# Optimization experiments

Measured on AMD Instinct MI355X. Metric: run time of the kernel, lower is better.

## Reference

```python
import jax, jax.numpy as jnp
import numpy as np

N, E = 50000, 800000          # nodes, edges (avg degree 16)
NFEAT, NHID, NCLASS = 256, 128, 64
HEADS = 4
P_DROP = 0.5


def setup_inputs() -> dict:
    key = jax.random.key(0)
    ks = jax.random.split(key, 12)

    def w(k, shape, fan_in):
        return jax.random.normal(k, shape, jnp.float32) * (1.0 / np.sqrt(fan_in))

    return {
        "features": jax.random.normal(ks[0], (N, NFEAT), jnp.float32),
        "src": jax.random.randint(ks[1], (E,), 0, N, jnp.int32),
        "dst": jax.random.randint(ks[2], (E,), 0, N, jnp.int32),
        # gc1: nfeat->nhid, 3 layers
        "wqkv1_0": w(ks[3], (3, NFEAT, NHID), NFEAT),
        "wqkv1_r": w(ks[4], (2, 3, NHID, NHID), NHID),
        "wo1": w(ks[5], (3, NHID, NHID), NHID),
        # gc2: nhid->nclass, 3 layers
        "wqkv2_0": w(ks[6], (3, NHID, NCLASS), NHID),
        "wqkv2_r": w(ks[7], (2, 3, NCLASS, NCLASS), NCLASS),
        "wo2": w(ks[8], (3, NCLASS, NCLASS), NCLASS),
        # gc3: nhid->nclass, 3 layers
        "wqkv3_0": w(ks[9], (3, NHID, NCLASS), NHID),
        "wqkv3_r": w(ks[10], (2, 3, NCLASS, NCLASS), NCLASS),
        "wo3": w(ks[11], (3, NCLASS, NCLASS), NCLASS),
    }


def _l2norm(x):
    # F.normalize(x): L2 along dim 1, eps=1e-12
    n = jnp.sqrt(jnp.sum(x * x, axis=1, keepdims=True))
    return x / jnp.maximum(n, 1e-12)


def _graph_transformer(h, src, dst, wqkv0, wqkvr, wo):
    """Stacked graph-transformer layers: gather q[dst]/k[src], edge-softmax per dst, scatter-sum v."""
    n = h.shape[0]
    n_layers = wo.shape[0]
    for l in range(n_layers):  # fixed small structural loop
        w = wqkv0 if l == 0 else wqkvr[l - 1]
        out_dim = w.shape[2]
        dh = out_dim // HEADS
        q = (h @ w[0]).reshape(n, HEADS, dh)
        k = (h @ w[1]).reshape(n, HEADS, dh)
        v = (h @ w[2]).reshape(n, HEADS, dh)
        # per-edge attention scores [E, H]
        s = jnp.einsum('ehd,ehd->eh', q[dst], k[src]) / np.sqrt(dh).astype(np.float32)
        # edge softmax over incoming edges of each dst node
        m = jax.ops.segment_max(s, dst, num_segments=n)
        e = jnp.exp(s - m[dst])
        denom = jax.ops.segment_sum(e, dst, num_segments=n)
        alpha = e / denom[dst]
        agg = jax.ops.segment_sum(alpha[:, :, None] * v[src], dst, num_segments=n)
        h = agg.reshape(n, out_dim) @ wo[l]
        if l < n_layers - 1:
            h = jax.nn.relu(h)
    return h


def reference(features, src, dst, wqkv1_0, wqkv1_r, wo1,
              wqkv2_0, wqkv2_r, wo2, wqkv3_0, wqkv3_r, wo3):
    key = jax.random.key(42)
    kd, ke = jax.random.split(key)

    x = _graph_transformer(features, src, dst, wqkv1_0, wqkv1_r, wo1)
    x = jax.nn.relu(_l2norm(x))
    # dropout (training=True), deterministic key
    keep = jax.random.bernoulli(kd, 1.0 - P_DROP, x.shape)
    x = jnp.where(keep, x / (1.0 - P_DROP), 0.0)

    mu = _l2norm(_graph_transformer(x, src, dst, wqkv2_0, wqkv2_r, wo2))
    logvar = _l2norm(_graph_transformer(x, src, dst, wqkv3_0, wqkv3_r, wo3))

    # reparameterize (training): std = exp(logvar) + 1e-12 (matches source exactly)
    std = jnp.exp(logvar) + 1e-12
    eps = jax.random.normal(ke, std.shape, std.dtype)
    z = eps * std + mu
    return z
```

## Files before the change

### kernel.cpp

```cpp
#include <hip/hip_runtime.h>
#include <stdint.h>
#include <math.h>

#define NN 50000
#define NE 800000
#define NH 4

typedef __attribute__((ext_vector_type(8))) short short8;
typedef __attribute__((ext_vector_type(4))) float floatx4;

__device__ inline float bf2f(uint32_t u16)
{
    return __uint_as_float(u16 << 16);
}
__device__ inline uint16_t f2bf(float f)
{
    uint32_t u = __float_as_uint(f);
    uint32_t r = (u + 0x7fffu + ((u >> 16) & 1u)) >> 16;
    return (uint16_t)r;
}
__device__ inline void unpk8(uint4 u, float* f)
{
    f[0] = bf2f(u.x & 0xffffu); f[1] = bf2f(u.x >> 16);
    f[2] = bf2f(u.y & 0xffffu); f[3] = bf2f(u.y >> 16);
    f[4] = bf2f(u.z & 0xffffu); f[5] = bf2f(u.z >> 16);
    f[6] = bf2f(u.w & 0xffffu); f[7] = bf2f(u.w >> 16);
}

__device__ inline void wave_lds_sync()
{
    __builtin_amdgcn_wave_barrier();
    asm volatile("s_waitcnt lgkmcnt(0)" ::: "memory");
    __builtin_amdgcn_wave_barrier();
}

__host__ __device__ inline void tf2x32(uint32_t k0, uint32_t k1,
                                       uint32_t x0, uint32_t x1,
                                       uint32_t& o0, uint32_t& o1)
{
    uint32_t ks2 = k0 ^ k1 ^ 0x1BD11BDAu;
    x0 += k0; x1 += k1;
#define TF_R(r) { x0 += x1; x1 = (x1 << (r)) | (x1 >> (32 - (r))); x1 ^= x0; }
    TF_R(13) TF_R(15) TF_R(26) TF_R(6)
    x0 += k1;  x1 += ks2 + 1u;
    TF_R(17) TF_R(29) TF_R(16) TF_R(24)
    x0 += ks2; x1 += k0 + 2u;
    TF_R(13) TF_R(15) TF_R(26) TF_R(6)
    x0 += k0;  x1 += k1 + 3u;
    TF_R(17) TF_R(29) TF_R(16) TF_R(24)
    x0 += k1;  x1 += ks2 + 4u;
    TF_R(13) TF_R(15) TF_R(26) TF_R(6)
    x0 += ks2; x1 += k0 + 5u;
#undef TF_R
    o0 = x0; o1 = x1;
}

__device__ inline uint32_t jax_bits32(uint32_t k0, uint32_t k1, uint32_t idx)
{
    uint32_t a, b;
    tf2x32(k0, k1, 0u, idx, a, b);
    return a ^ b;
}

__device__ inline float jax_u01(uint32_t bits)
{
    return __uint_as_float((bits >> 9) | 0x3f800000u) - 1.0f;
}

__device__ inline float erfinv_f(float x)
{
    float w = -log1pf(-x * x);
    float p;
    if (w < 5.0f) {
        w = w - 2.5f;
        p = 2.81022636e-08f;
        p = fmaf(p, w, 3.43273939e-07f);
        p = fmaf(p, w, -3.5233877e-06f);
        p = fmaf(p, w, -4.39150654e-06f);
        p = fmaf(p, w, 0.00021858087f);
        p = fmaf(p, w, -0.00125372503f);
        p = fmaf(p, w, -0.00417768164f);
        p = fmaf(p, w, 0.246640727f);
        p = fmaf(p, w, 1.50140941f);
    } else {
        w = sqrtf(w) - 3.0f;
        p = -0.000200214257f;
        p = fmaf(p, w, 0.000100950558f);
        p = fmaf(p, w, 0.00134934322f);
        p = fmaf(p, w, -0.00367342844f);
        p = fmaf(p, w, 0.00573950773f);
        p = fmaf(p, w, -0.0076224613f);
        p = fmaf(p, w, 0.00943887047f);
        p = fmaf(p, w, 1.00167406f);
        p = fmaf(p, w, 2.83297682f);
    }
    return p * x;
}

__global__ __launch_bounds__(256) void fill_u32_k(uint32_t* p, uint32_t v, int n)
{
    int i = blockIdx.x * blockDim.x + threadIdx.x;
    if (i < n) p[i] = v;
}

__global__ __launch_bounds__(256) void f2bf_vec_k(const float* __restrict__ in,
                                                  uint16_t* __restrict__ out, int n)
{
    int i = (blockIdx.x * blockDim.x + threadIdx.x) * 4;
    if (i >= n) return;
    float4 v = *(const float4*)(in + i);
    out[i + 0] = f2bf(v.x); out[i + 1] = f2bf(v.y);
    out[i + 2] = f2bf(v.z); out[i + 3] = f2bf(v.w);
}

struct WSeg { const float* src; int B, K, C, off; };
struct WSegs { WSeg s[18]; };

__global__ __launch_bounds__(256) void wconv_k(WSegs segs, uint16_t* __restrict__ Wt)
{
    WSeg sg = segs.s[blockIdx.y];
    int n = sg.B * sg.K * sg.C;
    int i = blockIdx.x * 256 + threadIdx.x;
    if (i >= n) return;
    int kc = sg.K * sg.C;
    int b = i / kc;
    int rr = i - b * kc;
    int k = rr / sg.C;
    int c = rr - k * sg.C;
    Wt[(size_t)sg.off + (size_t)(b * sg.C + c) * sg.K + k] = f2bf(sg.src[i]);
}

__global__ __launch_bounds__(256) void hist_k(const int* __restrict__ dst, int* __restrict__ deg)
{
    int e = blockIdx.x * blockDim.x + threadIdx.x;
    if (e < NE) atomicAdd(&deg[dst[e]], 1);
}

#define SCAN_CHUNK 1024
#define SCAN_NBLK  ((NN + SCAN_CHUNK - 1) / SCAN_CHUNK)

__global__ __launch_bounds__(256) void scan1_k(const int* __restrict__ deg,
                                               int* __restrict__ rowptr,
                                               int* __restrict__ bsums)
{
    __shared__ int lds[256];
    int b = blockIdx.x, t = threadIdx.x;
    int base = b * SCAN_CHUNK + t * 4;
    int v0 = (base + 0 < NN) ? deg[base + 0] : 0;
    int v1 = (base + 1 < NN) ? deg[base + 1] : 0;
    int v2 = (base + 2 < NN) ? deg[base + 2] : 0;
    int v3 = (base + 3 < NN) ? deg[base + 3] : 0;
    int s = v0 + v1 + v2 + v3;
    lds[t] = s;
    __syncthreads();
    for (int off = 1; off < 256; off <<= 1) {
        int x = (t >= off) ? lds[t - off] : 0;
        __syncthreads();
        lds[t] += x;
        __syncthreads();
    }
    int excl = lds[t] - s;
    if (base + 0 < NN) rowptr[base + 0] = excl;
    if (base + 1 < NN) rowptr[base + 1] = excl + v0;
    if (base + 2 < NN) rowptr[base + 2] = excl + v0 + v1;
    if (base + 3 < NN) rowptr[base + 3] = excl + v0 + v1 + v2;
    if (t == 255) bsums[b] = lds[255];
}

__global__ void scan2_k(int* bsums)
{
    if (threadIdx.x == 0 && blockIdx.x == 0) {
        int run = 0;
        for (int i = 0; i < SCAN_NBLK; i++) { int t = bsums[i]; bsums[i] = run; run += t; }
    }
}

__global__ __launch_bounds__(256) void scan3_k(int* __restrict__ rowptr,
                                               const int* __restrict__ bsums,
                                               int* __restrict__ cursor)
{
    int i = blockIdx.x * blockDim.x + threadIdx.x;
    if (i < NN) {
        int r = rowptr[i] + bsums[i / SCAN_CHUNK];
        rowptr[i] = r;
        cursor[i] = r;
    }
    if (i == 0) rowptr[NN] = NE;
}

__global__ __launch_bounds__(256) void csr_scatter_k(const int* __restrict__ src,
                                                     const int* __restrict__ dst,
                                                     int* __restrict__ cursor,
                                                     int* __restrict__ esrc)
{
    int e = blockIdx.x * blockDim.x + threadIdx.x;
    if (e >= NE) return;
    int d = dst[e];
    int pos = atomicAdd(&cursor[d], 1);
    esrc[pos] = src[e];
}

template<int K, int CH>
__global__ __launch_bounds__(256) void gemm_mfma_k(const uint16_t* __restrict__ A,
                                                   const uint16_t* __restrict__ Wt,
                                                   uint16_t* __restrict__ C,
                                                   int Ntot, int relu)
{
    constexpr int KP = K + 8;
    constexpr int KC = K / 8;
    constexpr int NT = CH / 16;
    extern __shared__ uint16_t smem[];
    uint16_t* As = smem;
    uint16_t* Ws = smem + 64 * KP;

    const int tid = threadIdx.x;
    const int row0 = blockIdx.x * 64;
    const int w  = tid >> 6;
    const int l  = tid & 63;
    const int lm = l & 15;
    const int lq = l >> 4;

    for (int i = tid; i < 64 * KC; i += 256) {
        int r = i / KC, c = i - r * KC;
        int gr = row0 + r; if (gr >= NN) gr = NN - 1;
        uint4 vv = *(const uint4*)(A + (size_t)gr * K + c * 8);
        *(uint4*)(As + r * KP + c * 8) = vv;
    }

    const uint16_t* a_base = As + (16 * w + lm) * KP + lq * 8;
    const uint16_t* b_base = Ws + lm * KP + lq * 8;

    const int nchunks = Ntot / CH;
    for (int ch = 0; ch < nchunks; ch++) {
        __syncthreads();
        for (int i = tid; i < CH * KC; i += 256) {
            int r = i / KC, c = i - r * KC;
            uint4 vv = *(const uint4*)(Wt + (size_t)(ch * CH + r) * K + c * 8);
            *(uint4*)(Ws + r * KP + c * 8) = vv;
        }
        __syncthreads();

        floatx4 acc[NT];
#pragma unroll
        for (int nt = 0; nt < NT; nt++) acc[nt] = (floatx4){0.f, 0.f, 0.f, 0.f};

#pragma unroll
        for (int ks = 0; ks < K / 32; ks++) {
            short8 av = *(const short8*)(a_base + ks * 32);
#pragma unroll
            for (int nt = 0; nt < NT; nt++) {
                short8 bv = *(const short8*)(b_base + nt * 16 * KP + ks * 32);
                acc[nt] = __builtin_amdgcn_mfma_f32_16x16x32_bf16(av, bv, acc[nt], 0, 0, 0);
            }
        }

        const int rbase = row0 + 16 * w + lq * 4;
        const int cbase = ch * CH + lm;
#pragma unroll
        for (int nt = 0; nt < NT; nt++) {
#pragma unroll
            for (int r = 0; r < 4; r++) {
                int gr = rbase + r;
                if (gr < NN) {
                    float v = acc[nt][r];
                    if (relu) v = fmaxf(v, 0.0f);
                    C[(size_t)gr * Ntot + cbase + nt * 16] = f2bf(v);
                }
            }
        }
    }
}

template<int DH>
__global__ __launch_bounds__(128) void attn_dual_k(const uint16_t* __restrict__ qkv,
                                                   const int* __restrict__ rowptr,
                                                   const int* __restrict__ esrc,
                                                   uint16_t* __restrict__ agg,
                                                   float scale)
{
    constexpr int OD  = NH * DH;
    constexpr int STR = 3 * OD;
    constexpr int QU  = DH / 8;
    constexpr int CAP = 64;
    constexpr int NP  = CAP / 16;
    constexpr int FV  = OD / 16;

    __shared__ float s_sc[2][CAP][4];
    __shared__ int   s_sn[2][CAP];

    const int wv   = threadIdx.x >> 6;
    const int lane = threadIdx.x & 63;
    const int n    = blockIdx.x * 2 + wv;
    const int h1   = lane & 3;
    const int e    = lane >> 2;
    const int g    = lane >> 4;
    const int dl   = lane & 15;
    const int h2   = dl >> 2;

    float qf[DH];
    {
        const uint4* q4 = (const uint4*)(qkv + (size_t)n * STR + h1 * DH);
#pragma unroll
        for (int i = 0; i < QU; i++) { uint4 u = q4[i]; unpk8(u, &qf[i * 8]); }
    }

    const int j0 = rowptr[n], j1 = rowptr[n + 1];

    float m = -INFINITY, l = 0.0f;
    float acc[FV];
#pragma unroll
    for (int i = 0; i < FV; i++) acc[i] = 0.0f;

    const int voff = 2 * OD + dl * FV;

    for (int c0 = j0; c0 < j1; c0 += CAP) {
        const int cn = min(j1 - c0, CAP);

        if (lane < cn) s_sn[wv][lane] = esrc[c0 + lane];
        wave_lds_sync();

        float p[NP];
        float lm = -INFINITY;
#pragma unroll
        for (int t = 0; t < NP; t++) {
            const int j = e + 16 * t;
            float s = -INFINITY;
            if (j < cn) {
                const int sn = s_sn[wv][j];
                const uint4* kp = (const uint4*)(qkv + (size_t)sn * STR + OD + h1 * DH);
                s = 0.0f;
#pragma unroll
                for (int i = 0; i < QU; i++) {
                    uint4 u = kp[i];
                    float kf[8];
                    unpk8(u, kf);
                    s = fmaf(qf[i * 8 + 0], kf[0], s); s = fmaf(qf[i * 8 + 1], kf[1], s);
                    s = fmaf(qf[i * 8 + 2], kf[2], s); s = fmaf(qf[i * 8 + 3], kf[3], s);
                    s = fmaf(qf[i * 8 + 4], kf[4], s); s = fmaf(qf[i * 8 + 5], kf[5], s);
                    s = fmaf(qf[i * 8 + 6], kf[6], s); s = fmaf(qf[i * 8 + 7], kf[7], s);
                }
                s *= scale;
            }
            p[t] = s;
            lm = fmaxf(lm, s);
        }
#pragma unroll
        for (int msk = 4; msk <= 32; msk <<= 1) lm = fmaxf(lm, __shfl_xor(lm, msk, 64));
        const float mn = fmaxf(m, lm);
        const float corr = expf(m - mn);
        m = mn;

        float ls = 0.0f;
#pragma unroll
        for (int t = 0; t < NP; t++) {
            const int j = e + 16 * t;
            float pe = 0.0f;
            if (j < cn) {
                pe = expf(p[t] - mn);
                s_sc[wv][j][h1] = pe;
            }
            ls += pe;
        }
#pragma unroll
        for (int msk = 4; msk <= 32; msk <<= 1) ls += __shfl_xor(ls, msk, 64);
        l = l * corr + ls;
        wave_lds_sync();

        const float c2 = __shfl(corr, h2, 64);
#pragma unroll
        for (int i = 0; i < FV; i++) acc[i] *= c2;

        for (int jb = 0; jb < cn; jb += 4) {
            const int j = jb + g;
            if (j < cn) {
                const float alpha = s_sc[wv][j][h2];
                const int sn = s_sn[wv][j];
                if constexpr (FV == 8) {
                    uint4 u = *(const uint4*)(qkv + (size_t)sn * STR + voff);
                    float vf[8];
                    unpk8(u, vf);
#pragma unroll
                    for (int i = 0; i < 8; i++) acc[i] = fmaf(alpha, vf[i], acc[i]);
                } else {
                    uint2 u = *(const uint2*)(qkv + (size_t)sn * STR + voff);
                    acc[0] = fmaf(alpha, bf2f(u.x & 0xffffu), acc[0]);
                    acc[1] = fmaf(alpha, bf2f(u.x >> 16),     acc[1]);
                    acc[2] = fmaf(alpha, bf2f(u.y & 0xffffu), acc[2]);
                    acc[3] = fmaf(alpha, bf2f(u.y >> 16),     acc[3]);
                }
            }
        }
        wave_lds_sync();
    }

    const float lh = __shfl(l, h2, 64);
    const float inv = (lh > 0.0f) ? 1.0f / lh : 0.0f;
#pragma unroll
    for (int i = 0; i < FV; i++) {
        acc[i] += __shfl_xor(acc[i], 16, 64);
        acc[i] += __shfl_xor(acc[i], 32, 64);
    }
    if (g == 0) {
        uint16_t* op = agg + (size_t)n * OD + dl * FV;
        uint32_t wword[FV / 2];
#pragma unroll
        for (int i = 0; i < FV / 2; i++)
            wword[i] = (uint32_t)f2bf(acc[2 * i] * inv) | ((uint32_t)f2bf(acc[2 * i + 1] * inv) << 16);
        if constexpr (FV == 8) {
            *(uint4*)op = make_uint4(wword[0], wword[1], wword[2], wword[3]);
        } else {
            *(uint2*)op = make_uint2(wword[0], wword[1]);
        }
    }
}

__global__ __launch_bounds__(256) void norm_relu_drop_k(const uint16_t* __restrict__ in,
                                                        uint16_t* __restrict__ out,
                                                        uint32_t k0, uint32_t k1)
{
    int row = blockIdx.x * 4 + (threadIdx.x >> 6);
    int lane = threadIdx.x & 63;
    if (row >= NN) return;
    const uint16_t* r = in + (size_t)row * 128;
    float a = bf2f(r[lane]), b = bf2f(r[lane + 64]);
    float ss = fmaf(a, a, b * b);
#pragma unroll
    for (int m = 32; m > 0; m >>= 1) ss += __shfl_xor(ss, m, 64);
    float d = fmaxf(sqrtf(ss), 1e-12f);
    float ya = fmaxf(a / d, 0.0f);
    float yb = fmaxf(b / d, 0.0f);
    uint32_t ia = (uint32_t)row * 128u + (uint32_t)lane;
    float ua = jax_u01(jax_bits32(k0, k1, ia));
    float ub = jax_u01(jax_bits32(k0, k1, ia + 64u));
    uint16_t* o = out + (size_t)row * 128;
    o[lane]      = f2bf((ua < 0.5f) ? ya * 2.0f : 0.0f);
    o[lane + 64] = f2bf((ub < 0.5f) ? yb * 2.0f : 0.0f);
}

__global__ __launch_bounds__(256) void norm64_k(const uint16_t* __restrict__ in,
                                                float* __restrict__ out)
{
    int row = blockIdx.x * 4 + (threadIdx.x >> 6);
    int lane = threadIdx.x & 63;
    if (row >= NN) return;
    float a = bf2f(in[(size_t)row * 64 + lane]);
    float ss = a * a;
#pragma unroll
    for (int m = 32; m > 0; m >>= 1) ss += __shfl_xor(ss, m, 64);
    float d = fmaxf(sqrtf(ss), 1e-12f);
    out[(size_t)row * 64 + lane] = a / d;
}

__global__ __launch_bounds__(256) void final_z_k(const float* __restrict__ mu,
                                                 const float* __restrict__ lv,
                                                 float* __restrict__ out,
                                                 uint32_t k0, uint32_t k1)
{
    int i = blockIdx.x * blockDim.x + threadIdx.x;
    if (i >= NN * 64) return;
    const float LO = -0.99999994f;
    float u01 = jax_u01(jax_bits32(k0, k1, (uint32_t)i));
    float u = fmaxf(LO, fmaf(u01, 2.0f, LO));
    float eps = 1.41421354f * erfinv_f(u);
    float stdv = expf(lv[i]) + 1e-12f;
    out[i] = fmaf(eps, stdv, mu[i]);
}

struct Bufs {
    uint16_t* Wt;
    uint16_t* feat_bf;
    uint16_t* qkv;
    uint16_t* agg;
    uint16_t* h1;
    uint16_t* h2;
    uint16_t* x;
    float* mu;
    float* lv;
    int* rowptr;
    int* cursor;
    int* bsums;
    int* esrc;
};

static void gemm_launch(int K, const uint16_t* A, const uint16_t* Wt, uint16_t* C,
                        int Ntot, int relu, hipStream_t s)
{
    int grid = (NN + 63) / 64;
    switch (K) {
    case 256: {
        size_t lds = (size_t)(64 + 32) * (256 + 8) * 2;
        gemm_mfma_k<256, 32><<<grid, 256, lds, s>>>(A, Wt, C, Ntot, relu);
        break;
    }
    case 128: {
        size_t lds = (size_t)(64 + 64) * (128 + 8) * 2;
        gemm_mfma_k<128, 64><<<grid, 256, lds, s>>>(A, Wt, C, Ntot, relu);
        break;
    }
    default: {
        size_t lds = (size_t)(64 + 64) * (64 + 8) * 2;
        gemm_mfma_k<64, 64><<<grid, 256, lds, s>>>(A, Wt, C, Ntot, relu);
        break;
    }
    }
}

static void run_gt_layer(const uint16_t* h_in, int K, int od,
                         const uint16_t* wqkv_t, const uint16_t* wo_t, bool relu,
                         uint16_t* h_out, const Bufs& B, hipStream_t stream)
{
    const int dh = od / NH;
    const float scale = 1.0f / sqrtf((float)dh);

    gemm_launch(K, h_in, wqkv_t, B.qkv, 3 * od, 0, stream);

    if (dh == 32)
        attn_dual_k<32><<<NN / 2, 128, 0, stream>>>(B.qkv, B.rowptr, B.esrc, B.agg, scale);
    else
        attn_dual_k<16><<<NN / 2, 128, 0, stream>>>(B.qkv, B.rowptr, B.esrc, B.agg, scale);

    gemm_launch(od, B.agg, wo_t, h_out, od, relu ? 1 : 0, stream);
}

extern "C" void kernel_launch(void* const* d_in, const int* in_sizes, int n_in,
                              void* d_out, int out_size, void* d_ws, size_t ws_size,
                              hipStream_t stream)
{
    const float* feat    = (const float*)d_in[0];
    const int*   src     = (const int*)d_in[1];
    const int*   dst     = (const int*)d_in[2];
    const float* wqkv1_0 = (const float*)d_in[3];
    const float* wqkv1_r = (const float*)d_in[4];
    const float* wo1     = (const float*)d_in[5];
    const float* wqkv2_0 = (const float*)d_in[6];
    const float* wqkv2_r = (const float*)d_in[7];
    const float* wo2     = (const float*)d_in[8];
    const float* wqkv3_0 = (const float*)d_in[9];
    const float* wqkv3_r = (const float*)d_in[10];
    const float* wo3     = (const float*)d_in[11];
    float* out = (float*)d_out;

    char* wp = (char*)d_ws;
    auto alloc = [&](size_t bytes) { char* p = wp; wp += (bytes + 255) & ~(size_t)255; return p; };

    WSegs segs;
    int offs[18];
    int acc_off = 0;
    auto seg = [&](int i, const float* p, int Bc, int Kc, int Cc) {
        segs.s[i].src = p; segs.s[i].B = Bc; segs.s[i].K = Kc; segs.s[i].C = Cc;
        segs.s[i].off = acc_off; offs[i] = acc_off; acc_off += Bc * Kc * Cc;
    };
    seg(0,  wqkv1_0,                 3, 256, 128);
    seg(1,  wqkv1_r,                 3, 128, 128);
    seg(2,  wqkv1_r + 3 * 128 * 128, 3, 128, 128);
    seg(3,  wo1,                     1, 128, 128);
    seg(4,  wo1 + 128 * 128,         1, 128, 128);
    seg(5,  wo1 + 2 * 128 * 128,     1, 128, 128);
    seg(6,  wqkv2_0,                 3, 128, 64);
    seg(7,  wqkv2_r,                 3, 64, 64);
    seg(8,  wqkv2_r + 3 * 64 * 64,   3, 64, 64);
    seg(9,  wo2,                     1, 64, 64);
    seg(10, wo2 + 64 * 64,           1, 64, 64);
    seg(11, wo2 + 2 * 64 * 64,       1, 64, 64);
    seg(12, wqkv3_0,                 3, 128, 64);
    seg(13, wqkv3_r,                 3, 64, 64);
    seg(14, wqkv3_r + 3 * 64 * 64,   3, 64, 64);
    seg(15, wo3,                     1, 64, 64);
    seg(16, wo3 + 64 * 64,           1, 64, 64);
    seg(17, wo3 + 2 * 64 * 64,       1, 64, 64);

    Bufs B;
    B.Wt      = (uint16_t*)alloc((size_t)acc_off * 2);
    B.feat_bf = (uint16_t*)alloc((size_t)NN * 256 * 2);
    B.qkv     = (uint16_t*)alloc((size_t)NN * 384 * 2);
    B.agg     = (uint16_t*)alloc((size_t)NN * 128 * 2);
    B.h1      = (uint16_t*)alloc((size_t)NN * 128 * 2);
    B.h2      = (uint16_t*)alloc((size_t)NN * 128 * 2);
    B.x       = (uint16_t*)alloc((size_t)NN * 128 * 2);
    B.mu      = (float*)alloc((size_t)NN * 64 * 4);
    B.lv      = (float*)alloc((size_t)NN * 64 * 4);
    B.rowptr  = (int*)alloc((size_t)(NN + 1) * 4);
    B.cursor  = (int*)alloc((size_t)NN * 4);
    B.bsums   = (int*)alloc((size_t)SCAN_NBLK * 4);
    B.esrc    = (int*)alloc((size_t)NE * 4);

    wconv_k<<<dim3(384, 18), 256, 0, stream>>>(segs, B.Wt);
    f2bf_vec_k<<<(NN * 256 / 4 + 255) / 256, 256, 0, stream>>>(feat, B.feat_bf, NN * 256);

    fill_u32_k<<<(NN + 255) / 256, 256, 0, stream>>>((uint32_t*)B.cursor, 0u, NN);
    hist_k<<<(NE + 255) / 256, 256, 0, stream>>>(dst, B.cursor);
    scan1_k<<<SCAN_NBLK, 256, 0, stream>>>(B.cursor, B.rowptr, B.bsums);
    scan2_k<<<1, 64, 0, stream>>>(B.bsums);
    scan3_k<<<(NN + 255) / 256, 256, 0, stream>>>(B.rowptr, B.bsums, B.cursor);
    csr_scatter_k<<<(NE + 255) / 256, 256, 0, stream>>>(src, dst, B.cursor, B.esrc);

    uint32_t kd0, kd1, ke0, ke1;
    tf2x32(0u, 42u, 0u, 0u, kd0, kd1);
    tf2x32(0u, 42u, 0u, 1u, ke0, ke1);

    run_gt_layer(B.feat_bf, 256, 128, B.Wt + offs[0], B.Wt + offs[3], true,  B.h1, B, stream);
    run_gt_layer(B.h1,      128, 128, B.Wt + offs[1], B.Wt + offs[4], true,  B.h2, B, stream);
    run_gt_layer(B.h2,      128, 128, B.Wt + offs[2], B.Wt + offs[5], false, B.h1, B, stream);

    norm_relu_drop_k<<<NN / 4, 256, 0, stream>>>(B.h1, B.x, kd0, kd1);

    run_gt_layer(B.x,  128, 64, B.Wt + offs[6], B.Wt + offs[9],  true,  B.h1, B, stream);
    run_gt_layer(B.h1, 64,  64, B.Wt + offs[7], B.Wt + offs[10], true,  B.h2, B, stream);
    run_gt_layer(B.h2, 64,  64, B.Wt + offs[8], B.Wt + offs[11], false, B.h1, B, stream);
    norm64_k<<<NN / 4, 256, 0, stream>>>(B.h1, B.mu);

    run_gt_layer(B.x,  128, 64, B.Wt + offs[12], B.Wt + offs[15], true,  B.h1, B, stream);
    run_gt_layer(B.h1, 64,  64, B.Wt + offs[13], B.Wt + offs[16], true,  B.h2, B, stream);
    run_gt_layer(B.h2, 64,  64, B.Wt + offs[14], B.Wt + offs[17], false, B.h1, B, stream);
    norm64_k<<<NN / 4, 256, 0, stream>>>(B.h1, B.lv);

    final_z_k<<<(NN * 64 + 255) / 256, 256, 0, stream>>>(B.mu, B.lv, out, ke0, ke1);
}
```

Baseline: 898.5 us.

## Batch mu/logvar branches via grid.y, fuse feature conversion and final normalization

Runs the mu and logvar graph-transformer branches together: both first-layer QKV projections share one GEMM over the reordered weight segments, and the later GEMMs and attention kernels process both branches through a second grid dimension. The fp32-to-bf16 feature conversion moves into the first GEMM's A-tile load, and the two norm64 kernels plus final_z are merged into one kernel. GEMM column chunks are widened (CH=128/192) so each block reloads its A tile fewer times. The intent is fewer launches, less intermediate traffic and larger grids, at the cost of more LDS per block and extra buffers.

Result: faster. 858.7 us (-4.4%).

```diff
diff --git a/kernel.cpp b/kernel.cpp
--- a/kernel.cpp
+++ b/kernel.cpp
@@ -103,16 +103,6 @@
     if (i < n) p[i] = v;
 }
 
-__global__ __launch_bounds__(256) void f2bf_vec_k(const float* __restrict__ in,
-                                                  uint16_t* __restrict__ out, int n)
-{
-    int i = (blockIdx.x * blockDim.x + threadIdx.x) * 4;
-    if (i >= n) return;
-    float4 v = *(const float4*)(in + i);
-    out[i + 0] = f2bf(v.x); out[i + 1] = f2bf(v.y);
-    out[i + 2] = f2bf(v.z); out[i + 3] = f2bf(v.w);
-}
-
 struct WSeg { const float* src; int B, K, C, off; };
 struct WSegs { WSeg s[18]; };
 
@@ -200,11 +190,11 @@
     esrc[pos] = src[e];
 }
 
-template<int K, int CH>
-__global__ __launch_bounds__(256) void gemm_mfma_k(const uint16_t* __restrict__ A,
-                                                   const uint16_t* __restrict__ Wt,
-                                                   uint16_t* __restrict__ C,
-                                                   int Ntot, int relu)
+struct GArg { const void* A; const uint16_t* W; uint16_t* C; };
+struct GArgs2 { GArg a[2]; };
+
+template<int K, int CH, bool AF32>
+__global__ __launch_bounds__(256) void gemm_mfma_k(GArgs2 gs, int Ntot, int relu)
 {
     constexpr int KP = K + 8;
     constexpr int KC = K / 8;
@@ -213,6 +203,10 @@
     uint16_t* As = smem;
     uint16_t* Ws = smem + 64 * KP;
 
+    const GArg g = gs.a[blockIdx.y];
+    const uint16_t* W = g.W;
+    uint16_t* C = g.C;
+
     const int tid = threadIdx.x;
     const int row0 = blockIdx.x * 64;
     const int w  = tid >> 6;
@@ -223,8 +217,20 @@
     for (int i = tid; i < 64 * KC; i += 256) {
         int r = i / KC, c = i - r * KC;
         int gr = row0 + r; if (gr >= NN) gr = NN - 1;
-        uint4 vv = *(const uint4*)(A + (size_t)gr * K + c * 8);
-        *(uint4*)(As + r * KP + c * 8) = vv;
+        if constexpr (AF32) {
+            const float* Af = (const float*)g.A + (size_t)gr * K + c * 8;
+            float4 f0 = *(const float4*)Af;
+            float4 f1 = *(const float4*)(Af + 4);
+            uint4 vv;
+            vv.x = (uint32_t)f2bf(f0.x) | ((uint32_t)f2bf(f0.y) << 16);
+            vv.y = (uint32_t)f2bf(f0.z) | ((uint32_t)f2bf(f0.w) << 16);
+            vv.z = (uint32_t)f2bf(f1.x) | ((uint32_t)f2bf(f1.y) << 16);
+            vv.w = (uint32_t)f2bf(f1.z) | ((uint32_t)f2bf(f1.w) << 16);
+            *(uint4*)(As + r * KP + c * 8) = vv;
+        } else {
+            uint4 vv = *(const uint4*)((const uint16_t*)g.A + (size_t)gr * K + c * 8);
+            *(uint4*)(As + r * KP + c * 8) = vv;
+        }
     }
 
     const uint16_t* a_base = As + (16 * w + lm) * KP + lq * 8;
@@ -235,7 +241,7 @@
         __syncthreads();
         for (int i = tid; i < CH * KC; i += 256) {
             int r = i / KC, c = i - r * KC;
-            uint4 vv = *(const uint4*)(Wt + (size_t)(ch * CH + r) * K + c * 8);
+            uint4 vv = *(const uint4*)(W + (size_t)(ch * CH + r) * K + c * 8);
             *(uint4*)(Ws + r * KP + c * 8) = vv;
         }
         __syncthreads();
@@ -271,15 +277,16 @@
     }
 }
 
+struct AArg { const uint16_t* qkv; uint16_t* agg; };
+struct AArgs2 { AArg a[2]; };
+
 template<int DH>
-__global__ __launch_bounds__(128) void attn_dual_k(const uint16_t* __restrict__ qkv,
+__global__ __launch_bounds__(128) void attn_dual_k(AArgs2 as,
                                                    const int* __restrict__ rowptr,
                                                    const int* __restrict__ esrc,
-                                                   uint16_t* __restrict__ agg,
-                                                   float scale)
+                                                   float scale, int str)
 {
     constexpr int OD  = NH * DH;
-    constexpr int STR = 3 * OD;
     constexpr int QU  = DH / 8;
     constexpr int CAP = 64;
     constexpr int NP  = CAP / 16;
@@ -287,6 +294,9 @@
 
     __shared__ float s_sc[2][CAP][4];
     __shared__ int   s_sn[2][CAP];
+
+    const uint16_t* qkv = as.a[blockIdx.y].qkv;
+    uint16_t* agg       = as.a[blockIdx.y].agg;
 
     const int wv   = threadIdx.x >> 6;
     const int lane = threadIdx.x & 63;
@@ -299,7 +309,7 @@
 
     float qf[DH];
     {
-        const uint4* q4 = (const uint4*)(qkv + (size_t)n * STR + h1 * DH);
+        const uint4* q4 = (const uint4*)(qkv + (size_t)n * str + h1 * DH);
 #pragma unroll
         for (int i = 0; i < QU; i++) { uint4 u = q4[i]; unpk8(u, &qf[i * 8]); }
     }
@@ -327,7 +337,7 @@
             float s = -INFINITY;
             if (j < cn) {
                 const int sn = s_sn[wv][j];
-                const uint4* kp = (const uint4*)(qkv + (size_t)sn * STR + OD + h1 * DH);
+                const uint4* kp = (const uint4*)(qkv + (size_t)sn * str + OD + h1 * DH);
                 s = 0.0f;
 #pragma unroll
                 for (int i = 0; i < QU; i++) {
@@ -376,13 +386,13 @@
                 const float alpha = s_sc[wv][j][h2];
                 const int sn = s_sn[wv][j];
                 if constexpr (FV == 8) {
-                    uint4 u = *(const uint4*)(qkv + (size_t)sn * STR + voff);
+                    uint4 u = *(const uint4*)(qkv + (size_t)sn * str + voff);
                     float vf[8];
                     unpk8(u, vf);
 #pragma unroll
                     for (int i = 0; i < 8; i++) acc[i] = fmaf(alpha, vf[i], acc[i]);
                 } else {
-                    uint2 u = *(const uint2*)(qkv + (size_t)sn * STR + voff);
+                    uint2 u = *(const uint2*)(qkv + (size_t)sn * str + voff);
                     acc[0] = fmaf(alpha, bf2f(u.x & 0xffffu), acc[0]);
                     acc[1] = fmaf(alpha, bf2f(u.x >> 16),     acc[1]);
                     acc[2] = fmaf(alpha, bf2f(u.y & 0xffffu), acc[2]);
@@ -437,89 +447,34 @@
     o[lane + 64] = f2bf((ub < 0.5f) ? yb * 2.0f : 0.0f);
 }
 
-__global__ __launch_bounds__(256) void norm64_k(const uint16_t* __restrict__ in,
-                                                float* __restrict__ out)
+__global__ __launch_bounds__(256) void final_fused_k(const uint16_t* __restrict__ hmu,
+                                                     const uint16_t* __restrict__ hlv,
+                                                     float* __restrict__ out,
+                                                     uint32_t k0, uint32_t k1)
 {
     int row = blockIdx.x * 4 + (threadIdx.x >> 6);
     int lane = threadIdx.x & 63;
     if (row >= NN) return;
-    float a = bf2f(in[(size_t)row * 64 + lane]);
-    float ss = a * a;
-#pragma unroll
-    for (int m = 32; m > 0; m >>= 1) ss += __shfl_xor(ss, m, 64);
-    float d = fmaxf(sqrtf(ss), 1e-12f);
-    out[(size_t)row * 64 + lane] = a / d;
-}
-
-__global__ __launch_bounds__(256) void final_z_k(const float* __restrict__ mu,
-                                                 const float* __restrict__ lv,
-                                                 float* __restrict__ out,
-                                                 uint32_t k0, uint32_t k1)
-{
-    int i = blockIdx.x * blockDim.x + threadIdx.x;
-    if (i >= NN * 64) return;
+    const size_t idx = (size_t)row * 64 + lane;
+
+    float a = bf2f(hmu[idx]);
+    float sa = a * a;
+#pragma unroll
+    for (int m = 32; m > 0; m >>= 1) sa += __shfl_xor(sa, m, 64);
+    float mu = a / fmaxf(sqrtf(sa), 1e-12f);
+
+    float b = bf2f(hlv[idx]);
+    float sb = b * b;
+#pragma unroll
+    for (int m = 32; m > 0; m >>= 1) sb += __shfl_xor(sb, m, 64);
+    float lv = b / fmaxf(sqrtf(sb), 1e-12f);
+
     const float LO = -0.99999994f;
-    float u01 = jax_u01(jax_bits32(k0, k1, (uint32_t)i));
+    float u01 = jax_u01(jax_bits32(k0, k1, (uint32_t)idx));
     float u = fmaxf(LO, fmaf(u01, 2.0f, LO));
     float eps = 1.41421354f * erfinv_f(u);
-    float stdv = expf(lv[i]) + 1e-12f;
-    out[i] = fmaf(eps, stdv, mu[i]);
-}
-
-struct Bufs {
-    uint16_t* Wt;
-    uint16_t* feat_bf;
-    uint16_t* qkv;
-    uint16_t* agg;
-    uint16_t* h1;
-    uint16_t* h2;
-    uint16_t* x;
-    float* mu;
-    float* lv;
-    int* rowptr;
-    int* cursor;
-    int* bsums;
-    int* esrc;
-};
-
-static void gemm_launch(int K, const uint16_t* A, const uint16_t* Wt, uint16_t* C,
-                        int Ntot, int relu, hipStream_t s)
-{
-    int grid = (NN + 63) / 64;
-    switch (K) {
-    case 256: {
-        size_t lds = (size_t)(64 + 32) * (256 + 8) * 2;
-        gemm_mfma_k<256, 32><<<grid, 256, lds, s>>>(A, Wt, C, Ntot, relu);
-        break;
-    }
-    case 128: {
-        size_t lds = (size_t)(64 + 64) * (128 + 8) * 2;
-        gemm_mfma_k<128, 64><<<grid, 256, lds, s>>>(A, Wt, C, Ntot, relu);
-        break;
-    }
-    default: {
-        size_t lds = (size_t)(64 + 64) * (64 + 8) * 2;
-        gemm_mfma_k<64, 64><<<grid, 256, lds, s>>>(A, Wt, C, Ntot, relu);
-        break;
-    }
-    }
-}
-
-static void run_gt_layer(const uint16_t* h_in, int K, int od,
-                         const uint16_t* wqkv_t, const uint16_t* wo_t, bool relu,
-                         uint16_t* h_out, const Bufs& B, hipStream_t stream)
-{
-    const int dh = od / NH;
-    const float scale = 1.0f / sqrtf((float)dh);
-
-    gemm_launch(K, h_in, wqkv_t, B.qkv, 3 * od, 0, stream);
-
-    if (dh == 32)
-        attn_dual_k<32><<<NN / 2, 128, 0, stream>>>(B.qkv, B.rowptr, B.esrc, B.agg, scale);
-    else
-        attn_dual_k<16><<<NN / 2, 128, 0, stream>>>(B.qkv, B.rowptr, B.esrc, B.agg, scale);
-
-    gemm_launch(od, B.agg, wo_t, h_out, od, relu ? 1 : 0, stream);
+    float stdv = expf(lv) + 1e-12f;
+    out[idx] = fmaf(eps, stdv, mu);
 }
 
 extern "C" void kernel_launch(void* const* d_in, const int* in_sizes, int n_in,
@@ -557,62 +512,104 @@
     seg(4,  wo1 + 128 * 128,         1, 128, 128);
     seg(5,  wo1 + 2 * 128 * 128,     1, 128, 128);
     seg(6,  wqkv2_0,                 3, 128, 64);
-    seg(7,  wqkv2_r,                 3, 64, 64);
-    seg(8,  wqkv2_r + 3 * 64 * 64,   3, 64, 64);
-    seg(9,  wo2,                     1, 64, 64);
-    seg(10, wo2 + 64 * 64,           1, 64, 64);
-    seg(11, wo2 + 2 * 64 * 64,       1, 64, 64);
-    seg(12, wqkv3_0,                 3, 128, 64);
-    seg(13, wqkv3_r,                 3, 64, 64);
-    seg(14, wqkv3_r + 3 * 64 * 64,   3, 64, 64);
+    seg(7,  wqkv3_0,                 3, 128, 64);
+    seg(8,  wqkv2_r,                 3, 64, 64);
+    seg(9,  wqkv3_r,                 3, 64, 64);
+    seg(10, wqkv2_r + 3 * 64 * 64,   3, 64, 64);
+    seg(11, wqkv3_r + 3 * 64 * 64,   3, 64, 64);
+    seg(12, wo2,                     1, 64, 64);
+    seg(13, wo2 + 64 * 64,           1, 64, 64);
+    seg(14, wo2 + 2 * 64 * 64,       1, 64, 64);
     seg(15, wo3,                     1, 64, 64);
     seg(16, wo3 + 64 * 64,           1, 64, 64);
     seg(17, wo3 + 2 * 64 * 64,       1, 64, 64);
 
-    Bufs B;
-    B.Wt      = (uint16_t*)alloc((size_t)acc_off * 2);
-    B.feat_bf = (uint16_t*)alloc((size_t)NN * 256 * 2);
-    B.qkv     = (uint16_t*)alloc((size_t)NN * 384 * 2);
-    B.agg     = (uint16_t*)alloc((size_t)NN * 128 * 2);
-    B.h1      = (uint16_t*)alloc((size_t)NN * 128 * 2);
-    B.h2      = (uint16_t*)alloc((size_t)NN * 128 * 2);
-    B.x       = (uint16_t*)alloc((size_t)NN * 128 * 2);
-    B.mu      = (float*)alloc((size_t)NN * 64 * 4);
-    B.lv      = (float*)alloc((size_t)NN * 64 * 4);
-    B.rowptr  = (int*)alloc((size_t)(NN + 1) * 4);
-    B.cursor  = (int*)alloc((size_t)NN * 4);
-    B.bsums   = (int*)alloc((size_t)SCAN_NBLK * 4);
-    B.esrc    = (int*)alloc((size_t)NE * 4);
-
-    wconv_k<<<dim3(384, 18), 256, 0, stream>>>(segs, B.Wt);
-    f2bf_vec_k<<<(NN * 256 / 4 + 255) / 256, 256, 0, stream>>>(feat, B.feat_bf, NN * 256);
-
-    fill_u32_k<<<(NN + 255) / 256, 256, 0, stream>>>((uint32_t*)B.cursor, 0u, NN);
-    hist_k<<<(NE + 255) / 256, 256, 0, stream>>>(dst, B.cursor);
-    scan1_k<<<SCAN_NBLK, 256, 0, stream>>>(B.cursor, B.rowptr, B.bsums);
-    scan2_k<<<1, 64, 0, stream>>>(B.bsums);
-    scan3_k<<<(NN + 255) / 256, 256, 0, stream>>>(B.rowptr, B.bsums, B.cursor);
-    csr_scatter_k<<<(NE + 255) / 256, 256, 0, stream>>>(src, dst, B.cursor, B.esrc);
+    uint16_t* Wt     = (uint16_t*)alloc((size_t)acc_off * 2);
+    uint16_t* qkvL   = (uint16_t*)alloc((size_t)NN * 384 * 2);
+    uint16_t* agg128 = (uint16_t*)alloc((size_t)NN * 128 * 2);
+    uint16_t* h1     = (uint16_t*)alloc((size_t)NN * 128 * 2);
+    uint16_t* h2     = (uint16_t*)alloc((size_t)NN * 128 * 2);
+    uint16_t* x      = (uint16_t*)alloc((size_t)NN * 128 * 2);
+    uint16_t* qkv_mu = (uint16_t*)alloc((size_t)NN * 192 * 2);
+    uint16_t* qkv_lv = (uint16_t*)alloc((size_t)NN * 192 * 2);
+    uint16_t* agg_mu = (uint16_t*)alloc((size_t)NN * 64 * 2);
+    uint16_t* agg_lv = (uint16_t*)alloc((size_t)NN * 64 * 2);
+    uint16_t* hmu    = (uint16_t*)alloc((size_t)NN * 64 * 2);
+    uint16_t* hlv    = (uint16_t*)alloc((size_t)NN * 64 * 2);
+    uint16_t* hmu2   = (uint16_t*)alloc((size_t)NN * 64 * 2);
+    uint16_t* hlv2   = (uint16_t*)alloc((size_t)NN * 64 * 2);
+    int* rowptr = (int*)alloc((size_t)(NN + 1) * 4);
+    int* cursor = (int*)alloc((size_t)NN * 4);
+    int* bsums  = (int*)alloc((size_t)SCAN_NBLK * 4);
+    int* esrc   = (int*)alloc((size_t)NE * 4);
+
+    wconv_k<<<dim3(384, 18), 256, 0, stream>>>(segs, Wt);
+
+    fill_u32_k<<<(NN + 255) / 256, 256, 0, stream>>>((uint32_t*)cursor, 0u, NN);
+    hist_k<<<(NE + 255) / 256, 256, 0, stream>>>(dst, cursor);
+    scan1_k<<<SCAN_NBLK, 256, 0, stream>>>(cursor, rowptr, bsums);
+    scan2_k<<<1, 64, 0, stream>>>(bsums);
+    scan3_k<<<(NN + 255) / 256, 256, 0, stream>>>(rowptr, bsums, cursor);
+    csr_scatter_k<<<(NE + 255) / 256, 256, 0, stream>>>(src, dst, cursor, esrc);
 
     uint32_t kd0, kd1, ke0, ke1;
     tf2x32(0u, 42u, 0u, 0u, kd0, kd1);
     tf2x32(0u, 42u, 0u, 1u, ke0, ke1);
 
-    run_gt_layer(B.feat_bf, 256, 128, B.Wt + offs[0], B.Wt + offs[3], true,  B.h1, B, stream);
-    run_gt_layer(B.h1,      128, 128, B.Wt + offs[1], B.Wt + offs[4], true,  B.h2, B, stream);
-    run_gt_layer(B.h2,      128, 128, B.Wt + offs[2], B.Wt + offs[5], false, B.h1, B, stream);
-
-    norm_relu_drop_k<<<NN / 4, 256, 0, stream>>>(B.h1, B.x, kd0, kd1);
-
-    run_gt_layer(B.x,  128, 64, B.Wt + offs[6], B.Wt + offs[9],  true,  B.h1, B, stream);
-    run_gt_layer(B.h1, 64,  64, B.Wt + offs[7], B.Wt + offs[10], true,  B.h2, B, stream);
-    run_gt_layer(B.h2, 64,  64, B.Wt + offs[8], B.Wt + offs[11], false, B.h1, B, stream);
-    norm64_k<<<NN / 4, 256, 0, stream>>>(B.h1, B.mu);
-
-    run_gt_layer(B.x,  128, 64, B.Wt + offs[12], B.Wt + offs[15], true,  B.h1, B, stream);
-    run_gt_layer(B.h1, 64,  64, B.Wt + offs[13], B.Wt + offs[16], true,  B.h2, B, stream);
-    run_gt_layer(B.h2, 64,  64, B.Wt + offs[14], B.Wt + offs[17], false, B.h1, B, stream);
-    norm64_k<<<NN / 4, 256, 0, stream>>>(B.h1, B.lv);
-
-    final_z_k<<<(NN * 64 + 255) / 256, 256, 0, stream>>>(B.mu, B.lv, out, ke0, ke1);
-}
+    const int GX = (NN + 63) / 64;
+    const float sc32 = 1.0f / sqrtf(32.0f);
+    const float sc16 = 0.25f;
+
+    auto g1 = [&](GArg a) { GArgs2 g; g.a[0] = a; g.a[1] = a; return g; };
+    auto g2 = [&](GArg a0, GArg a1) { GArgs2 g; g.a[0] = a0; g.a[1] = a1; return g; };
+    auto a1 = [&](AArg a) { AArgs2 r; r.a[0] = a; r.a[1] = a; return r; };
+    auto a2 = [&](AArg a0, AArg b0) { AArgs2 r; r.a[0] = a0; r.a[1] = b0; return r; };
+
+    const size_t L256_32  = (size_t)(64 + 32)  * (256 + 8) * 2;
+    const size_t L128_128 = (size_t)(64 + 128) * (128 + 8) * 2;
+    const size_t L64_192  = (size_t)(64 + 192) * (64 + 8) * 2;
+    const size_t L64_64   = (size_t)(64 + 64)  * (64 + 8) * 2;
+
+    gemm_mfma_k<256, 32, true><<<dim3(GX, 1), 256, L256_32, stream>>>(
+        g1({feat, Wt + offs[0], qkvL}), 384, 0);
+    attn_dual_k<32><<<dim3(NN / 2, 1), 128, 0, stream>>>(a1({qkvL, agg128}), rowptr, esrc, sc32, 384);
+    gemm_mfma_k<128, 128, false><<<dim3(GX, 1), 256, L128_128, stream>>>(
+        g1({agg128, Wt + offs[3], h1}), 128, 1);
+
+    gemm_mfma_k<128, 128, false><<<dim3(GX, 1), 256, L128_128, stream>>>(
+        g1({h1, Wt + offs[1], qkvL}), 384, 0);
+    attn_dual_k<32><<<dim3(NN / 2, 1), 128, 0, stream>>>(a1({qkvL, agg128}), rowptr, esrc, sc32, 384);
+    gemm_mfma_k<128, 128, false><<<dim3(GX, 1), 256, L128_128, stream>>>(
+        g1({agg128, Wt + offs[4], h2}), 128, 1);
+
+    gemm_mfma_k<128, 128, false><<<dim3(GX, 1), 256, L128_128, stream>>>(
+        g1({h2, Wt + offs[2], qkvL}), 384, 0);
+    attn_dual_k<32><<<dim3(NN / 2, 1), 128, 0, stream>>>(a1({qkvL, agg128}), rowptr, esrc, sc32, 384);
+    gemm_mfma_k<128, 128, false><<<dim3(GX, 1), 256, L128_128, stream>>>(
+        g1({agg128, Wt + offs[5], h1}), 128, 0);
+
+    norm_relu_drop_k<<<NN / 4, 256, 0, stream>>>(h1, x, kd0, kd1);
+
+    gemm_mfma_k<128, 128, false><<<dim3(GX, 1), 256, L128_128, stream>>>(
+        g1({x, Wt + offs[6], qkvL}), 384, 0);
+    attn_dual_k<16><<<dim3(NN / 2, 2), 128, 0, stream>>>(
+        a2({qkvL, agg_mu}, {qkvL + 192, agg_lv}), rowptr, esrc, sc16, 384);
+    gemm_mfma_k<64, 64, false><<<dim3(GX, 2), 256, L64_64, stream>>>(
+        g2({agg_mu, Wt + offs[12], hmu}, {agg_lv, Wt + offs[15], hlv}), 64, 1);
+
+    gemm_mfma_k<64, 192, false><<<dim3(GX, 2), 256, L64_192, stream>>>(
+        g2({hmu, Wt + offs[8], qkv_mu}, {hlv, Wt + offs[9], qkv_lv}), 192, 0);
+    attn_dual_k<16><<<dim3(NN / 2, 2), 128, 0, stream>>>(
+        a2({qkv_mu, agg_mu}, {qkv_lv, agg_lv}), rowptr, esrc, sc16, 192);
+    gemm_mfma_k<64, 64, false><<<dim3(GX, 2), 256, L64_64, stream>>>(
+        g2({agg_mu, Wt + offs[13], hmu2}, {agg_lv, Wt + offs[16], hlv2}), 64, 1);
+
+    gemm_mfma_k<64, 192, false><<<dim3(GX, 2), 256, L64_192, stream>>>(
+        g2({hmu2, Wt + offs[10], qkv_mu}, {hlv2, Wt + offs[11], qkv_lv}), 192, 0);
+    attn_dual_k<16><<<dim3(NN / 2, 2), 128, 0, stream>>>(
+        a2({qkv_mu, agg_mu}, {qkv_lv, agg_lv}), rowptr, esrc, sc16, 192);
+    gemm_mfma_k<64, 64, false><<<dim3(GX, 2), 256, L64_64, stream>>>(
+        g2({agg_mu, Wt + offs[14], hmu}, {agg_lv, Wt + offs[17], hlv}), 64, 0);
+
+    final_fused_k<<<NN / 4, 256, 0, stream>>>(hmu, hlv, out, ke0, ke1);
+}
```
